# Kernel optimization log

Hardware: AMD Instinct MI355X
Metric: run time of the kernel (lower is better)

## Reference

```python
import jax, jax.numpy as jnp
import numpy as np

B, N = 2, 1024
D, H, DK, L = 128, 8, 16, 4
K_GCN, K_LOC, COARSE = 16, 8, 512
EPS = 1e-5
SCALE = 1.0 / float(np.sqrt(DK))


def _dist2(q, r):
    # squared euclidean distances [Nq, Nr]; same ordering as torch.cdist for topk
    return jnp.sum(q * q, -1)[:, None] - 2.0 * (q @ r.T) + jnp.sum(r * r, -1)[None, :]


def _knn_self(coords, k):
    # knn_graph(loop=False): k nearest neighbors excluding self, per batch
    def one(c):
        d2 = _dist2(c, c) + jnp.eye(c.shape[0], dtype=c.dtype) * 1e10
        return jax.lax.top_k(-d2, k)[1]  # [N, k] source-node indices
    return jax.vmap(one)(coords)


def _gcn(x, idx, w, b, k):
    # PyG GCNConv with self-loops on a knn graph: target in-degree is uniformly k+1,
    # so gcn_norm reduces to mean over {self} U knn neighbors.
    nb = jax.vmap(lambda xb, ib: xb[ib])(x, idx)  # [B,N,k,C]
    agg = (x + nb.sum(2)) / float(k + 1)
    return agg @ w + b


def _ln(x, g, b):
    m = x.mean(-1, keepdims=True)
    v = ((x - m) ** 2).mean(-1, keepdims=True)
    return (x - m) * jax.lax.rsqrt(v + EPS) * g + b


def _neigh_mean(part, pred, k):
    # local_knn + mean over the k gathered partial neighbors
    def one(pb, qb):
        idx = jax.lax.top_k(-_dist2(qb, pb), k)[1]  # [Nq,k]
        return pb[idx].mean(1)                      # [Nq,3]
    return jax.vmap(one)(part, pred)


def _refine(part, pred, sw1, sb1, sw2, sb2, dw, db, cw, cb):
    # LocalRefineStage: seed MLP -> ConvTranspose1d(k=2,s=2) on length-1 seq -> 1x1 conv -> offsets
    nm = _neigh_mean(part, pred, K_LOC)
    comb = jnp.concatenate([pred, nm], -1)                          # [B,N,6]
    seed = jax.nn.relu(comb @ sw1 + sb1) @ sw2 + sb2                # [B,N,128]
    h = jax.nn.relu(jnp.einsum('bnc,cot->bnot', seed, dw) + db[:, None])  # [B,N,128,2]
    y = jnp.einsum('bnot,po->bntp', h, cw) + cb                     # [B,N,2,3]
    child = pred[:, :, None, :] + y
    return child.reshape(pred.shape[0], -1, 3)


def _forward(partial_coords, gcn_w0, gcn_b0, gcn_w1, gcn_b1, enc_fw, enc_fb,
             t_wq, t_bq, t_wk, t_bk, t_wv, t_bv, t_alpha,
             t_f1w, t_f1b, t_f2w, t_f2b, t_ln1g, t_ln1b, t_ln2g, t_ln2b,
             dec_w1, dec_b1, dec_w2, dec_b2,
             st_sw1, st_sb1, st_sw2, st_sb2, st_dw, st_db, st_cw, st_cb):
    coords = partial_coords
    # --- GraphEncoder ---
    idx = _knn_self(coords, K_GCN)
    x = jax.nn.relu(_gcn(coords, idx, gcn_w0, gcn_b0, K_GCN))
    x = jax.nn.relu(_gcn(x, idx, gcn_w1, gcn_b1, K_GCN))
    x = x @ enc_fw + enc_fb  # tokens [B,N,128]; bridge_in is Identity (128==128)
    # --- GeomMultiTokenTransformer ---
    # block-diagonal extraction of (coords coords^T) == per-batch dot-product bias
    G = jnp.einsum('bnc,bmc->bnm', coords, coords)
    for i in range(L):
        q = (x @ t_wq[i] + t_bq[i]).reshape(B, N, H, DK)
        k = (x @ t_wk[i] + t_bk[i]).reshape(B, N, H, DK)
        v = (x @ t_wv[i] + t_bv[i]).reshape(B, N, H, DK)
        scores = jnp.einsum('bnhd,bmhd->bhnm', q, k) * SCALE + (t_alpha[i] * G)[:, None]
        a = jax.nn.softmax(scores, axis=-1)
        attn = jnp.einsum('bhnm,bmhd->bnhd', a, v).reshape(B, N, D)
        x = _ln(x + attn, t_ln1g[i], t_ln1b[i])
        ff = jax.nn.relu(x @ t_f1w[i] + t_f1b[i]) @ t_f2w[i] + t_f2b[i]
        x = _ln(x + ff, t_ln2g[i], t_ln2b[i])
    # --- Snowflake3StageDecoder ---
    gc = x.mean(1)
    pts = (jax.nn.relu(gc @ dec_w1 + dec_b1) @ dec_w2 + dec_b2).reshape(B, COARSE, 3)
    for s in range(3):
        pts = _refine(coords, pts, st_sw1[s], st_sb1[s], st_sw2[s], st_sb2[s],
                      st_dw[s], st_db[s], st_cw[s], st_cb[s])
    return pts  # [B, 4096, 3]


def setup_inputs() -> dict:
    key = jax.random.key(0)
    it = iter(jax.random.split(key, 64))
    def w(*shape):
        return jax.random.normal(next(it), shape, dtype=jnp.float32) * 0.05
    z = lambda *s: jnp.zeros(s, dtype=jnp.float32)
    o = lambda *s: jnp.ones(s, dtype=jnp.float32)
    return {
        'partial_coords': jax.random.normal(next(it), (B, N, 3), dtype=jnp.float32),
        'gcn_w0': w(3, 64), 'gcn_b0': z(64),
        'gcn_w1': w(64, 128), 'gcn_b1': z(128),
        'enc_fw': w(128, 128), 'enc_fb': z(128),
        't_wq': w(L, D, D), 't_bq': z(L, D),
        't_wk': w(L, D, D), 't_bk': z(L, D),
        't_wv': w(L, D, D), 't_bv': z(L, D),
        't_alpha': jnp.full((L,), 0.1, dtype=jnp.float32),
        't_f1w': w(L, D, 4 * D), 't_f1b': z(L, 4 * D),
        't_f2w': w(L, 4 * D, D), 't_f2b': z(L, D),
        't_ln1g': o(L, D), 't_ln1b': z(L, D),
        't_ln2g': o(L, D), 't_ln2b': z(L, D),
        'dec_w1': w(128, 128), 'dec_b1': z(128),
        'dec_w2': w(128, 3 * COARSE), 'dec_b2': z(3 * COARSE),
        'st_sw1': w(3, 6, 128), 'st_sb1': z(3, 128),
        'st_sw2': w(3, 128, 128), 'st_sb2': z(3, 128),
        'st_dw': w(3, 128, 128, 2), 'st_db': z(3, 128),
        'st_cw': w(3, 3, 128), 'st_cb': z(3, 3),
    }


def reference(partial_coords, gcn_w0, gcn_b0, gcn_w1, gcn_b1, enc_fw, enc_fb,
              t_wq, t_bq, t_wk, t_bk, t_wv, t_bv, t_alpha,
              t_f1w, t_f1b, t_f2w, t_f2b, t_ln1g, t_ln1b, t_ln2g, t_ln2b,
              dec_w1, dec_b1, dec_w2, dec_b2,
              st_sw1, st_sb1, st_sw2, st_sb2, st_dw, st_db, st_cw, st_cb):
    return _forward(partial_coords, gcn_w0, gcn_b0, gcn_w1, gcn_b1, enc_fw, enc_fb,
                    t_wq, t_bq, t_wk, t_bk, t_wv, t_bv, t_alpha,
                    t_f1w, t_f1b, t_f2w, t_f2b, t_ln1g, t_ln1b, t_ln2g, t_ln2b,
                    dec_w1, dec_b1, dec_w2, dec_b2,
                    st_sw1, st_sb1, st_sw2, st_sb2, st_dw, st_db, st_cw, st_cb)
```

## Files before the change

### kernel.cpp

```cpp
#include <hip/hip_runtime.h>


#define B_ 2
#define N_ 1024
#define D_ 128
#define H_ 8
#define DK_ 16
#define L_ 4
#define KG_ 16
#define KLOC_ 8
#define COARSE_ 512
#define AW_ 8
#define KSP_ 4
#define PREC_ 17
#define QPL_ 4

static __device__ __forceinline__ float wave_sum(float v) {
    #pragma unroll
    for (int off = 32; off > 0; off >>= 1) v += __shfl_xor(v, off);
    return v;
}
static __device__ __forceinline__ float half_sum(float v) {
    #pragma unroll
    for (int off = 16; off > 0; off >>= 1) v += __shfl_xor(v, off);
    return v;
}

template <int CIN, bool RELU, bool BIAS_HALF>
static __device__ __forceinline__ float4 gemm_body(
        const float* __restrict__ X, const float* __restrict__ W,
        const float* __restrict__ bias, int wstride, int col0) {
    __shared__ float Xs[8 * CIN];
    __shared__ float Ws[64][128];
    int tid = threadIdx.x;
    int row0 = blockIdx.x * 8;
    constexpr int NX4 = 2 * CIN;
    {
        const float4* xg = (const float4*)(X + (size_t)row0 * CIN);
        float4* xs4 = (float4*)Xs;
        #pragma unroll
        for (int i = 0; i < (NX4 + 255) / 256; ++i) {
            int t = tid + i * 256;
            if ((NX4 % 256 == 0) || t < NX4) xs4[t] = xg[t];
        }
    }
    int col4 = (tid & 31) << 2;
    int rowl = tid >> 5;
    float4 acc;
    if (BIAS_HALF) {
        acc.x = bias[(col0 + col4) >> 1];
        acc.y = bias[(col0 + col4 + 1) >> 1];
        acc.z = bias[(col0 + col4 + 2) >> 1];
        acc.w = bias[(col0 + col4 + 3) >> 1];
    } else {
        acc = *(const float4*)(bias + col0 + col4);
    }
    for (int c0 = 0; c0 < CIN; c0 += 64) {
        __syncthreads();
        #pragma unroll
        for (int i = 0; i < 8; ++i) {
            int flat = tid + i * 256;
            int wr = flat >> 5, wc = (flat & 31) << 2;
            *(float4*)&Ws[wr][wc] =
                *(const float4*)(W + (size_t)(c0 + wr) * wstride + col0 + wc);
        }
        __syncthreads();
        const float* xrow = Xs + rowl * CIN + c0;
        #pragma unroll
        for (int c = 0; c < 64; ++c) {
            float xv = xrow[c];
            float4 w = *(const float4*)&Ws[c][col4];
            acc.x += xv * w.x; acc.y += xv * w.y;
            acc.z += xv * w.z; acc.w += xv * w.w;
        }
    }
    if (RELU) {
        acc.x = fmaxf(acc.x, 0.f); acc.y = fmaxf(acc.y, 0.f);
        acc.z = fmaxf(acc.z, 0.f); acc.w = fmaxf(acc.w, 0.f);
    }
    return acc;
}

template <int CIN, bool RELU, bool BIAS_HALF>
__global__ __launch_bounds__(256) void gemm128_kernel(
        const float* __restrict__ X, const float* __restrict__ W,
        const float* __restrict__ bias, float* __restrict__ Y,
        int wstride, int ystride) {
    int col0 = blockIdx.y * 128;
    float4 acc = gemm_body<CIN, RELU, BIAS_HALF>(X, W, bias, wstride, col0);
    int col4 = (threadIdx.x & 31) << 2;
    int row = blockIdx.x * 8 + (threadIdx.x >> 5);
    *(float4*)(Y + (size_t)row * ystride + col0 + col4) = acc;
}

template <int CIN>
__global__ __launch_bounds__(256) void gemm_ln_kernel(
        const float* __restrict__ X, const float* __restrict__ W,
        const float* __restrict__ bias, const float* __restrict__ res,
        const float* __restrict__ g, const float* __restrict__ bt,
        float* __restrict__ Y) {
    float4 acc = gemm_body<CIN, false, false>(X, W, bias, 128, 0);
    int col4 = (threadIdx.x & 31) << 2;
    int row = blockIdx.x * 8 + (threadIdx.x >> 5);
    float4 r = *(const float4*)(res + (size_t)row * D_ + col4);
    acc.x += r.x; acc.y += r.y; acc.z += r.z; acc.w += r.w;
    float mean = half_sum(acc.x + acc.y + acc.z + acc.w) * (1.0f / D_);
    float dx = acc.x - mean, dy = acc.y - mean, dz = acc.z - mean, dw = acc.w - mean;
    float var = half_sum(dx * dx + dy * dy + dz * dz + dw * dw) * (1.0f / D_);
    float rstd = rsqrtf(var + 1e-5f);
    float4 gv = *(const float4*)(g + col4);
    float4 bv = *(const float4*)(bt + col4);
    float4 o;
    o.x = dx * rstd * gv.x + bv.x;
    o.y = dy * rstd * gv.y + bv.y;
    o.z = dz * rstd * gv.z + bv.z;
    o.w = dw * rstd * gv.w + bv.w;
    *(float4*)(Y + (size_t)row * D_ + col4) = o;
}

__global__ __launch_bounds__(256) void gemm_ffn1_kernel(
        const float* __restrict__ pp, const float* __restrict__ xin,
        const float* __restrict__ g, const float* __restrict__ bt,
        const float* __restrict__ W, const float* __restrict__ bias,
        float* __restrict__ xln, float* __restrict__ Y) {
    __shared__ float Xs[8 * 128];
    __shared__ float Ws[64][128];
    int tid = threadIdx.x;
    int row0 = blockIdx.x * 8;
    int col0 = blockIdx.y * 128;
    int col4 = (tid & 31) << 2;
    int rowl = tid >> 5;
    {
        int row = row0 + rowl;
        int b = row >> 10, n = row & (N_ - 1);
        int h = col4 >> 4, d0 = col4 & 15;
        const float* p = pp + (((size_t)(b * 8 + h) * N_ + n) * KSP_) * PREC_;
        float gsum = 0.f, a0 = 0.f, a1 = 0.f, a2 = 0.f, a3 = 0.f;
        #pragma unroll
        for (int s = 0; s < KSP_; ++s) {
            const float* ps = p + s * PREC_;
            gsum += ps[0];
            a0 += ps[1 + d0]; a1 += ps[2 + d0]; a2 += ps[3 + d0]; a3 += ps[4 + d0];
        }
        float inv = 1.0f / gsum;
        float4 xv = *(const float4*)(xin + (size_t)row * D_ + col4);
        float v0 = a0 * inv + xv.x;
        float v1 = a1 * inv + xv.y;
        float v2 = a2 * inv + xv.z;
        float v3 = a3 * inv + xv.w;
        float mean = half_sum(v0 + v1 + v2 + v3) * (1.0f / D_);
        float dx = v0 - mean, dy = v1 - mean, dz = v2 - mean, dw = v3 - mean;
        float var = half_sum(dx * dx + dy * dy + dz * dz + dw * dw) * (1.0f / D_);
        float rstd = rsqrtf(var + 1e-5f);
        float4 gv = *(const float4*)(g + col4);
        float4 bv = *(const float4*)(bt + col4);
        float4 o;
        o.x = dx * rstd * gv.x + bv.x;
        o.y = dy * rstd * gv.y + bv.y;
        o.z = dz * rstd * gv.z + bv.z;
        o.w = dw * rstd * gv.w + bv.w;
        *(float4*)&Xs[rowl * 128 + col4] = o;
        if (blockIdx.y == 0)
            *(float4*)(xln + (size_t)row * D_ + col4) = o;
    }
    float4 acc = *(const float4*)(bias + col0 + col4);
    for (int c0 = 0; c0 < 128; c0 += 64) {
        __syncthreads();
        #pragma unroll
        for (int i = 0; i < 8; ++i) {
            int flat = tid + i * 256;
            int wr = flat >> 5, wc = (flat & 31) << 2;
            *(float4*)&Ws[wr][wc] =
                *(const float4*)(W + (size_t)(c0 + wr) * 512 + col0 + wc);
        }
        __syncthreads();
        const float* xrow = Xs + rowl * 128 + c0;
        #pragma unroll
        for (int c = 0; c < 64; ++c) {
            float xv = xrow[c];
            float4 w = *(const float4*)&Ws[c][col4];
            acc.x += xv * w.x; acc.y += xv * w.y;
            acc.z += xv * w.z; acc.w += xv * w.w;
        }
    }
    acc.x = fmaxf(acc.x, 0.f); acc.y = fmaxf(acc.y, 0.f);
    acc.z = fmaxf(acc.z, 0.f); acc.w = fmaxf(acc.w, 0.f);
    int row = row0 + rowl;
    *(float4*)(Y + (size_t)row * 512 + col0 + col4) = acc;
}

__global__ __launch_bounds__(256) void qkv3_kernel(
        const float* __restrict__ X,
        const float* __restrict__ Wq, const float* __restrict__ bq,
        const float* __restrict__ Wk, const float* __restrict__ bk,
        const float* __restrict__ Wv, const float* __restrict__ bv,
        float* __restrict__ Q, float* __restrict__ K, float* __restrict__ V) {
    const float* W; const float* bias; float* Y;
    if (blockIdx.y == 0)      { W = Wq; bias = bq; Y = Q; }
    else if (blockIdx.y == 1) { W = Wk; bias = bk; Y = K; }
    else                      { W = Wv; bias = bv; Y = V; }
    float4 acc = gemm_body<128, false, false>(X, W, bias, 128, 0);
    int col4 = (threadIdx.x & 31) << 2;
    int row = blockIdx.x * 8 + (threadIdx.x >> 5);
    int b = row >> 10, n = row & (N_ - 1);
    int h = col4 >> 4, d = col4 & 15;
    *(float4*)(Y + (((size_t)(b * 8 + h) * N_ + n) << 4) + d) = acc;
}

__global__ __launch_bounds__(256) void knn_fused_kernel(
        const float* __restrict__ coords, int* __restrict__ knn) {
    __shared__ float4 sc[N_];
    int wid = threadIdx.x >> 6;
    int lane = threadIdx.x & 63;
    size_t q = (size_t)blockIdx.x * 4 + wid;
    int b = (int)(q >> 10), n = (int)(q & (N_ - 1));
    const float* cb = coords + (size_t)b * N_ * 3;
    for (int i = threadIdx.x; i < N_; i += 256) {
        float x = cb[i * 3], y = cb[i * 3 + 1], z = cb[i * 3 + 2];
        sc[i] = make_float4(x, y, z, x * x + y * y + z * z);
    }
    __syncthreads();
    float4 qc = sc[n];
    float qx = qc.x, qy = qc.y, qz = qc.z, q2 = qc.w;
    float ld[16];
    #pragma unroll
    for (int j = 0; j < 16; ++j) {
        int m = (j << 6) | lane;
        float4 c = sc[m];
        float dot = qx * c.x + qy * c.y + qz * c.z;
        float d = (q2 - 2.0f * dot) + c.w;
        ld[j] = (m == n) ? 3e38f : d;
    }
    int* o = knn + q * KG_;
    #pragma unroll
    for (int r = 0; r < KG_; ++r) {
        float dm = ld[0]; int im = lane;
        #pragma unroll
        for (int j = 1; j < 16; ++j) {
            int mj = (j << 6) | lane;
            bool lt = (ld[j] < dm) || (ld[j] == dm && mj < im);
            dm = lt ? ld[j] : dm; im = lt ? mj : im;
        }
        #pragma unroll
        for (int off = 32; off > 0; off >>= 1) {
            float d2 = __shfl_xor(dm, off); int i2 = __shfl_xor(im, off);
            bool lt = (d2 < dm) || (d2 == dm && i2 < im);
            dm = lt ? d2 : dm; im = lt ? i2 : im;
        }
        if (lane == 0) o[r] = im;
        if ((im & 63) == lane) {
            #pragma unroll
            for (int j = 0; j < 16; ++j) if ((im >> 6) == j) ld[j] = 3e38f;
        }
    }
}

__global__ __launch_bounds__(256) void loc_fused_kernel(
        const float* __restrict__ part, const float* __restrict__ pred,
        const float* __restrict__ sw1, const float* __restrict__ sb1,
        float* __restrict__ seedh, int Nq) {
    __shared__ float4 sc[N_];
    int wid = threadIdx.x >> 6;
    int lane = threadIdx.x & 63;
    size_t q = (size_t)blockIdx.x * 4 + wid;
    int b = (int)(q / Nq);
    const float* pb = part + (size_t)b * N_ * 3;
    for (int i = threadIdx.x; i < N_; i += 256) {
        float x = pb[i * 3], y = pb[i * 3 + 1], z = pb[i * 3 + 2];
        sc[i] = make_float4(x, y, z, x * x + y * y + z * z);
    }
    __syncthreads();
    const float* pr = pred + q * 3;
    float qx = pr[0], qy = pr[1], qz = pr[2];
    float q2 = qx * qx + qy * qy + qz * qz;
    float ld[16];
    #pragma unroll
    for (int j = 0; j < 16; ++j) {
        int m = (j << 6) | lane;
        float4 c = sc[m];
        float dot = qx * c.x + qy * c.y + qz * c.z;
        ld[j] = (q2 - 2.0f * dot) + c.w;
    }
    float sx = 0.f, sy = 0.f, sz = 0.f;
    #pragma unroll
    for (int r = 0; r < KLOC_; ++r) {
        float dm = ld[0]; int im = lane;
        #pragma unroll
        for (int j = 1; j < 16; ++j) {
            int mj = (j << 6) | lane;
            bool lt = (ld[j] < dm) || (ld[j] == dm && mj < im);
            dm = lt ? ld[j] : dm; im = lt ? mj : im;
        }
        #pragma unroll
        for (int off = 32; off > 0; off >>= 1) {
            float d2 = __shfl_xor(dm, off); int i2 = __shfl_xor(im, off);
            bool lt = (d2 < dm) || (d2 == dm && i2 < im);
            dm = lt ? d2 : dm; im = lt ? i2 : im;
        }
        float4 w = sc[im];
        sx += w.x; sy += w.y; sz += w.z;
        if ((im & 63) == lane) {
            #pragma unroll
            for (int j = 0; j < 16; ++j) if ((im >> 6) == j) ld[j] = 3e38f;
        }
    }
    float comb[6];
    comb[0] = qx; comb[1] = qy; comb[2] = qz;
    comb[3] = sx * (1.0f / KLOC_);
    comb[4] = sy * (1.0f / KLOC_);
    comb[5] = sz * (1.0f / KLOC_);
    float* so = seedh + q * 128;
    #pragma unroll
    for (int half = 0; half < 2; ++half) {
        int c = lane + half * 64;
        float acc = sb1[c];
        #pragma unroll
        for (int i = 0; i < 6; ++i) acc += comb[i] * sw1[i * 128 + c];
        so[c] = fmaxf(acc, 0.f);
    }
}

__global__ void gcn_agg_kernel(const float* __restrict__ x,
                               const int* __restrict__ knn,
                               float* __restrict__ agg, int C) {
    int i = blockIdx.x * blockDim.x + threadIdx.x;
    if (i >= B_ * N_ * C) return;
    int c = i % C;
    int n = (i / C) % N_;
    int b = i / (C * N_);
    const int* id = knn + ((size_t)b * N_ + n) * KG_;
    float s = x[((size_t)b * N_ + n) * C + c];
    #pragma unroll
    for (int j = 0; j < KG_; ++j) s += x[((size_t)b * N_ + id[j]) * C + c];
    agg[i] = s * (1.0f / (KG_ + 1));
}

template <bool RELU>
__global__ void linear4_kernel(const float* __restrict__ X,
                               const float* __restrict__ W,
                               const float* __restrict__ bias,
                               float* __restrict__ Y,
                               int rows, int Cin, int Cout) {
    int co4 = Cout >> 2;
    int idx = blockIdx.x * blockDim.x + threadIdx.x;
    if (idx >= rows * co4) return;
    int r = idx / co4, o4 = (idx - r * co4) << 2;
    const float* x = X + (size_t)r * Cin;
    float4 acc = *(const float4*)(bias + o4);
    #pragma unroll 4
    for (int c = 0; c < Cin; ++c) {
        float xv = x[c];
        float4 w = *(const float4*)(W + (size_t)c * Cout + o4);
        acc.x += xv * w.x; acc.y += xv * w.y; acc.z += xv * w.z; acc.w += xv * w.w;
    }
    if (RELU) {
        acc.x = fmaxf(acc.x, 0.f); acc.y = fmaxf(acc.y, 0.f);
        acc.z = fmaxf(acc.z, 0.f); acc.w = fmaxf(acc.w, 0.f);
    }
    *(float4*)(Y + (size_t)r * Cout + o4) = acc;
}

__global__ __launch_bounds__(512) void attn_part(
        const float* __restrict__ q,
        const float* __restrict__ k,
        const float* __restrict__ v,
        const float* __restrict__ coords,
        const float* __restrict__ alphap, int layer,
        float* __restrict__ pp) {
    __shared__ float smem[10304];
    float* kst = smem;
    float* vst = smem + 4096;
    float* ssum = smem;
    float* sacc = smem + 2048;
    int bh = blockIdx.x & 15;
    int t = blockIdx.x >> 4;
    int ks = t & (KSP_ - 1);
    int nb = t >> 2;
    int b = bh >> 3;
    int wid = threadIdx.x >> 6;
    int lane = threadIdx.x & 63;
    float alpha = alphap[layer];
    {
        const float4* kg = (const float4*)(k + (((size_t)bh * N_ + ks * 256) << 4));
        const float4* vg = (const float4*)(v + (((size_t)bh * N_ + ks * 256) << 4));
        float4* ks4 = (float4*)kst;
        float4* vs4 = (float4*)vst;
        #pragma unroll
        for (int i = 0; i < 2; ++i) {
            int idx = threadIdx.x + i * 512;
            ks4[idx] = kg[idx];
            vs4[idx] = vg[idx];
        }
    }
    int n0 = nb * 256 + lane;
    const float* cb = coords + (size_t)b * N_ * 3;
    float qv[QPL_][DK_];
    float cx[QPL_], cy[QPL_], cz[QPL_];
    #pragma unroll
    for (int u = 0; u < QPL_; ++u) {
        const float* qp = q + (((size_t)bh * N_ + n0 + u * 64) << 4);
        #pragma unroll
        for (int d = 0; d < DK_; ++d) qv[u][d] = qp[d];
        int nn = n0 + u * 64;
        cx[u] = cb[nn * 3]; cy[u] = cb[nn * 3 + 1]; cz[u] = cb[nn * 3 + 2];
    }
    float sm[QPL_];
    float acc[QPL_][DK_];
    #pragma unroll
    for (int u = 0; u < QPL_; ++u) {
        sm[u] = 0.f;
        #pragma unroll
        for (int d = 0; d < DK_; ++d) acc[u][d] = 0.f;
    }
    __syncthreads();
    int mbase = ks * 256 + wid * 32;
    int lbase = wid * 32;
    #pragma unroll 2
    for (int j = 0; j < 32; ++j) {
        float kk[16];
        {
            const float4* kr = (const float4*)(kst + ((lbase + j) << 4));
            *(float4*)&kk[0] = kr[0]; *(float4*)&kk[4] = kr[1];
            *(float4*)&kk[8] = kr[2]; *(float4*)&kk[12] = kr[3];
        }
        int m = mbase + j;
        float wx = cb[m * 3], wy = cb[m * 3 + 1], wz = cb[m * 3 + 2];
        float p[QPL_];
        #pragma unroll
        for (int u = 0; u < QPL_; ++u) {
            float dot = 0.f;
            #pragma unroll
            for (int d = 0; d < DK_; ++d) dot += qv[u][d] * kk[d];
            p[u] = __expf(dot * 0.25f + alpha * (wx * cx[u] + wy * cy[u] + wz * cz[u]));
            sm[u] += p[u];
        }
        float vv[16];
        {
            const float4* vr = (const float4*)(vst + ((lbase + j) << 4));
            *(float4*)&vv[0] = vr[0]; *(float4*)&vv[4] = vr[1];
            *(float4*)&vv[8] = vr[2]; *(float4*)&vv[12] = vr[3];
        }
        #pragma unroll
        for (int u = 0; u < QPL_; ++u)
            #pragma unroll
            for (int d = 0; d < DK_; ++d) acc[u][d] += p[u] * vv[d];
    }
    __syncthreads();
    #pragma unroll
    for (int u = 0; u < QPL_; ++u) ssum[wid * 256 + u * 64 + lane] = sm[u];
    int qi = threadIdx.x & 63;
    int dq = threadIdx.x >> 6;
    #pragma unroll
    for (int r = 0; r < QPL_; ++r) {
        #pragma unroll
        for (int d = 0; d < DK_; ++d) sacc[lane * 129 + wid * DK_ + d] = acc[r][d];
        __syncthreads();
        int n = nb * 256 + r * 64 + qi;
        float* o = pp + (((size_t)bh * N_ + n) * KSP_ + ks) * PREC_;
        if (dq == 0) {
            float gsum = 0.f;
            #pragma unroll
            for (int w = 0; w < AW_; ++w) gsum += ssum[w * 256 + r * 64 + qi];
            o[0] = gsum;
        }
        #pragma unroll
        for (int dd = 0; dd < 2; ++dd) {
            int d = dq * 2 + dd;
            float a = 0.f;
            #pragma unroll
            for (int w = 0; w < AW_; ++w) a += sacc[qi * 129 + w * DK_ + d];
            o[1 + d] = a;
        }
        __syncthreads();
    }
}

__global__ void colmean_kernel(const float* __restrict__ x,
                               float* __restrict__ gc) {
    int b = blockIdx.x;
    int d = threadIdx.x & 127;
    int sl = threadIdx.x >> 7;
    __shared__ float part[4][128];
    float s = 0.f;
    const float* xb = x + (size_t)b * N_ * D_;
    for (int n = sl * 256; n < sl * 256 + 256; ++n) s += xb[(size_t)n * D_ + d];
    part[sl][d] = s;
    __syncthreads();
    if (sl == 0)
        gc[b * D_ + d] = (part[0][d] + part[1][d] + part[2][d] + part[3][d]) * (1.0f / N_);
}

__global__ void child_kernel(const float* __restrict__ h,
                             const float* __restrict__ cw,
                             const float* __restrict__ cb,
                             const float* __restrict__ pred,
                             float* __restrict__ outp, int Nq) {
    int idx = blockIdx.x * blockDim.x + threadIdx.x;
    if (idx >= B_ * Nq * 6) return;
    int p = idx % 3;
    int t = (idx / 3) & 1;
    int n = (idx / 6) % Nq;
    int b = idx / (6 * Nq);
    const float* hr = h + ((size_t)b * Nq + n) * 256;
    float acc = cb[p];
    #pragma unroll 4
    for (int o = 0; o < 128; ++o) acc += hr[o * 2 + t] * cw[p * 128 + o];
    outp[idx] = pred[((size_t)b * Nq + n) * 3 + p] + acc;
}

static inline int cdiv(int a, int b) { return (a + b - 1) / b; }

extern "C" void kernel_launch(void* const* d_in, const int* in_sizes, int n_in,
                              void* d_out, int out_size, void* d_ws, size_t ws_size,
                              hipStream_t stream) {
    (void)in_sizes; (void)n_in; (void)out_size; (void)ws_size;
    const float* coords = (const float*)d_in[0];
    const float* gcn_w0 = (const float*)d_in[1];
    const float* gcn_b0 = (const float*)d_in[2];
    const float* gcn_w1 = (const float*)d_in[3];
    const float* gcn_b1 = (const float*)d_in[4];
    const float* enc_fw = (const float*)d_in[5];
    const float* enc_fb = (const float*)d_in[6];
    const float* t_wq   = (const float*)d_in[7];
    const float* t_bq   = (const float*)d_in[8];
    const float* t_wk   = (const float*)d_in[9];
    const float* t_bk   = (const float*)d_in[10];
    const float* t_wv   = (const float*)d_in[11];
    const float* t_bv   = (const float*)d_in[12];
    const float* t_alpha= (const float*)d_in[13];
    const float* t_f1w  = (const float*)d_in[14];
    const float* t_f1b  = (const float*)d_in[15];
    const float* t_f2w  = (const float*)d_in[16];
    const float* t_f2b  = (const float*)d_in[17];
    const float* t_ln1g = (const float*)d_in[18];
    const float* t_ln1b = (const float*)d_in[19];
    const float* t_ln2g = (const float*)d_in[20];
    const float* t_ln2b = (const float*)d_in[21];
    const float* dec_w1 = (const float*)d_in[22];
    const float* dec_b1 = (const float*)d_in[23];
    const float* dec_w2 = (const float*)d_in[24];
    const float* dec_b2 = (const float*)d_in[25];
    const float* st_sw1 = (const float*)d_in[26];
    const float* st_sb1 = (const float*)d_in[27];
    const float* st_sw2 = (const float*)d_in[28];
    const float* st_sb2 = (const float*)d_in[29];
    const float* st_dw  = (const float*)d_in[30];
    const float* st_db  = (const float*)d_in[31];
    const float* st_cw  = (const float*)d_in[32];
    const float* st_cb  = (const float*)d_in[33];
    float* out = (float*)d_out;

    char* ws = (char*)d_ws;
    size_t off = 0;
    auto alloc = [&](size_t bytes) -> void* {
        void* p = ws + off;
        off += (bytes + 255) & ~(size_t)255;
        return p;
    };
    int*   knn   = (int*)  alloc((size_t)B_ * N_ * KG_ * 4);
    float* app   = (float*)alloc((size_t)B_ * H_ * N_ * KSP_ * PREC_ * 4);
    float* agg   = (float*)alloc((size_t)B_ * N_ * 64 * 4);
    float* x64   = (float*)alloc((size_t)B_ * N_ * 64 * 4);
    float* xb    = (float*)alloc((size_t)B_ * N_ * D_ * 4);
    float* x     = (float*)alloc((size_t)B_ * N_ * D_ * 4);
    float* q     = (float*)alloc((size_t)B_ * N_ * D_ * 4);
    float* k     = (float*)alloc((size_t)B_ * N_ * D_ * 4);
    float* v     = (float*)alloc((size_t)B_ * N_ * D_ * 4);
    float* ffh   = (float*)alloc((size_t)B_ * N_ * 512 * 4);
    float* gc    = (float*)alloc((size_t)B_ * D_ * 4);
    float* dech  = (float*)alloc((size_t)B_ * D_ * 4);
    float* pts0  = (float*)alloc((size_t)B_ * COARSE_ * 3 * 4);
    float* pts1  = (float*)alloc((size_t)B_ * 1024 * 3 * 4);
    float* pts2  = (float*)alloc((size_t)B_ * 2048 * 3 * 4);
    float* seedh = (float*)alloc((size_t)B_ * 2048 * 128 * 4);
    float* seed  = (float*)alloc((size_t)B_ * 2048 * 128 * 4);
    float* hb    = (float*)alloc((size_t)B_ * 2048 * 256 * 4);

    const int rows = B_ * N_;

    knn_fused_kernel<<<rows / 4, 256, 0, stream>>>(coords, knn);
    gcn_agg_kernel<<<cdiv(rows * 3, 256), 256, 0, stream>>>(coords, knn, agg, 3);
    linear4_kernel<true><<<cdiv(rows * 16, 256), 256, 0, stream>>>(agg, gcn_w0, gcn_b0, x64, rows, 3, 64);
    gcn_agg_kernel<<<cdiv(rows * 64, 256), 256, 0, stream>>>(x64, knn, agg, 64);
    gemm128_kernel<64, true, false><<<dim3(rows / 8, 1), 256, 0, stream>>>(agg, gcn_w1, gcn_b1, xb, 128, 128);
    gemm128_kernel<128, false, false><<<dim3(rows / 8, 1), 256, 0, stream>>>(xb, enc_fw, enc_fb, x, 128, 128);

    for (int i = 0; i < L_; ++i) {
        qkv3_kernel<<<dim3(rows / 8, 3), 256, 0, stream>>>(
            x, t_wq + i * 16384, t_bq + i * 128, t_wk + i * 16384, t_bk + i * 128,
            t_wv + i * 16384, t_bv + i * 128, q, k, v);
        attn_part<<<B_ * H_ * (N_ / 256) * KSP_, 512, 0, stream>>>(q, k, v, coords, t_alpha, i, app);
        gemm_ffn1_kernel<<<dim3(rows / 8, 4), 256, 0, stream>>>(
            app, x, t_ln1g + i * 128, t_ln1b + i * 128,
            t_f1w + i * 128 * 512, t_f1b + i * 512, xb, ffh);
        gemm_ln_kernel<512><<<rows / 8, 256, 0, stream>>>(ffh, t_f2w + i * 512 * 128, t_f2b + i * 128, xb, t_ln2g + i * 128, t_ln2b + i * 128, x);
    }

    colmean_kernel<<<B_, 512, 0, stream>>>(x, gc);
    linear4_kernel<true><<<cdiv(B_ * 32, 256), 256, 0, stream>>>(gc, dec_w1, dec_b1, dech, B_, 128, 128);
    linear4_kernel<false><<<cdiv(B_ * 384, 256), 256, 0, stream>>>(dech, dec_w2, dec_b2, pts0, B_, 128, 1536);

    const float* pred = pts0;
    float* outs[3] = { pts1, pts2, out };
    int Nq = COARSE_;
    for (int s = 0; s < 3; ++s) {
        int srows = B_ * Nq;
        loc_fused_kernel<<<srows / 4, 256, 0, stream>>>(
            coords, pred, st_sw1 + s * 6 * 128, st_sb1 + s * 128, seedh, Nq);
        gemm128_kernel<128, false, false><<<dim3(srows / 8, 1), 256, 0, stream>>>(seedh, st_sw2 + s * 128 * 128, st_sb2 + s * 128, seed, 128, 128);
        gemm128_kernel<128, true, true><<<dim3(srows / 8, 2), 256, 0, stream>>>(seed, st_dw + s * 128 * 256, st_db + s * 128, hb, 256, 256);
        child_kernel<<<cdiv(srows * 6, 256), 256, 0, stream>>>(hb, st_cw + s * 3 * 128, st_cb + s * 3, pred, outs[s], Nq);
        pred = outs[s];
        Nq <<= 1;
    }
}
```

Before: 422.4 us.

## Fuse GCN aggregation, decoder MLP and refine-stage tail into fewer kernels

Folds the GCN neighbor aggregation into the following linear layers: a per-row kernel for the 3-to-64 layer, and aggregation into shared memory ahead of the 64-to-128 GEMM. The two decoder linear layers merge into one kernel. The refine-stage 1x1 GEMM, transposed-conv GEMM and child offset computation become one kernel that keeps intermediates in shared memory. This removes many launches and global round trips for the agg, seed and hb buffers, at the cost of more shared memory per block and recomputing the decoder's first layer in every block.

```diff
diff --git a/kernel.cpp b/kernel.cpp
--- a/kernel.cpp
+++ b/kernel.cpp
@@ -91,6 +91,74 @@
     int col4 = (threadIdx.x & 31) << 2;
     int row = blockIdx.x * 8 + (threadIdx.x >> 5);
     *(float4*)(Y + (size_t)row * ystride + col0 + col4) = acc;
+}
+
+__global__ __launch_bounds__(256) void gemm_gcn_kernel(
+        const float* __restrict__ x64, const int* __restrict__ knn,
+        const float* __restrict__ W, const float* __restrict__ bias,
+        float* __restrict__ Y) {
+    __shared__ float Xs[8 * 64];
+    __shared__ float Ws[64][128];
+    int tid = threadIdx.x;
+    int row0 = blockIdx.x * 8;
+    #pragma unroll
+    for (int i = 0; i < 2; ++i) {
+        int idx = tid + i * 256;
+        int r = idx >> 6, c = idx & 63;
+        int row = row0 + r;
+        int b = row >> 10;
+        const int* id = knn + (size_t)row * KG_;
+        float val = x64[(size_t)row * 64 + c];
+        #pragma unroll
+        for (int j = 0; j < KG_; ++j)
+            val += x64[((size_t)(b << 10) + id[j]) * 64 + c];
+        Xs[idx] = val * (1.0f / (KG_ + 1));
+    }
+    int col4 = (tid & 31) << 2;
+    int rowl = tid >> 5;
+    float4 acc = *(const float4*)(bias + col4);
+    __syncthreads();
+    #pragma unroll
+    for (int i = 0; i < 8; ++i) {
+        int flat = tid + i * 256;
+        int wr = flat >> 5, wc = (flat & 31) << 2;
+        *(float4*)&Ws[wr][wc] = *(const float4*)(W + (size_t)wr * 128 + wc);
+    }
+    __syncthreads();
+    const float* xrow = Xs + rowl * 64;
+    #pragma unroll
+    for (int c = 0; c < 64; ++c) {
+        float xv = xrow[c];
+        float4 w = *(const float4*)&Ws[c][col4];
+        acc.x += xv * w.x; acc.y += xv * w.y;
+        acc.z += xv * w.z; acc.w += xv * w.w;
+    }
+    acc.x = fmaxf(acc.x, 0.f); acc.y = fmaxf(acc.y, 0.f);
+    acc.z = fmaxf(acc.z, 0.f); acc.w = fmaxf(acc.w, 0.f);
+    int row = row0 + rowl;
+    *(float4*)(Y + (size_t)row * 128 + col4) = acc;
+}
+
+__global__ __launch_bounds__(256) void gcnlin0_kernel(
+        const float* __restrict__ coords, const int* __restrict__ knn,
+        const float* __restrict__ w0, const float* __restrict__ b0,
+        float* __restrict__ x64) {
+    int lane = threadIdx.x & 63;
+    int row = blockIdx.x * 4 + (threadIdx.x >> 6);
+    int b = row >> 10;
+    const float* cb = coords + (size_t)(b << 10) * 3;
+    int n = row & (N_ - 1);
+    float ax = cb[n * 3], ay = cb[n * 3 + 1], az = cb[n * 3 + 2];
+    const int* id = knn + (size_t)row * KG_;
+    #pragma unroll
+    for (int j = 0; j < KG_; ++j) {
+        int m = id[j];
+        ax += cb[m * 3]; ay += cb[m * 3 + 1]; az += cb[m * 3 + 2];
+    }
+    float s = 1.0f / (KG_ + 1);
+    ax *= s; ay *= s; az *= s;
+    float acc = b0[lane] + ax * w0[lane] + ay * w0[64 + lane] + az * w0[128 + lane];
+    x64[(size_t)row * 64 + lane] = fmaxf(acc, 0.f);
 }
 
 template <int CIN>
@@ -320,44 +388,116 @@
     }
 }
 
-__global__ void gcn_agg_kernel(const float* __restrict__ x,
-                               const int* __restrict__ knn,
-                               float* __restrict__ agg, int C) {
-    int i = blockIdx.x * blockDim.x + threadIdx.x;
-    if (i >= B_ * N_ * C) return;
-    int c = i % C;
-    int n = (i / C) % N_;
-    int b = i / (C * N_);
-    const int* id = knn + ((size_t)b * N_ + n) * KG_;
-    float s = x[((size_t)b * N_ + n) * C + c];
-    #pragma unroll
-    for (int j = 0; j < KG_; ++j) s += x[((size_t)b * N_ + id[j]) * C + c];
-    agg[i] = s * (1.0f / (KG_ + 1));
-}
-
-template <bool RELU>
-__global__ void linear4_kernel(const float* __restrict__ X,
-                               const float* __restrict__ W,
-                               const float* __restrict__ bias,
-                               float* __restrict__ Y,
-                               int rows, int Cin, int Cout) {
-    int co4 = Cout >> 2;
-    int idx = blockIdx.x * blockDim.x + threadIdx.x;
-    if (idx >= rows * co4) return;
-    int r = idx / co4, o4 = (idx - r * co4) << 2;
-    const float* x = X + (size_t)r * Cin;
-    float4 acc = *(const float4*)(bias + o4);
+__global__ __launch_bounds__(256) void refine_tail_kernel(
+        const float* __restrict__ seedh,
+        const float* __restrict__ sw2, const float* __restrict__ sb2,
+        const float* __restrict__ dw, const float* __restrict__ db,
+        const float* __restrict__ cw, const float* __restrict__ cb,
+        const float* __restrict__ pred, float* __restrict__ outp) {
+    __shared__ float Xs[8 * 128];
+    __shared__ float Ws[64][128];
+    __shared__ float Sd[8 * 128];
+    __shared__ float Hb[8 * 256];
+    int tid = threadIdx.x;
+    int row0 = blockIdx.x * 8;
+    int col4 = (tid & 31) << 2;
+    int rowl = tid >> 5;
+    {
+        const float4* xg = (const float4*)(seedh + (size_t)row0 * 128);
+        float4* xs4 = (float4*)Xs;
+        xs4[tid] = xg[tid];
+    }
+    float4 acc = *(const float4*)(sb2 + col4);
+    for (int c0 = 0; c0 < 128; c0 += 64) {
+        __syncthreads();
+        #pragma unroll
+        for (int i = 0; i < 8; ++i) {
+            int flat = tid + i * 256;
+            int wr = flat >> 5, wc = (flat & 31) << 2;
+            *(float4*)&Ws[wr][wc] =
+                *(const float4*)(sw2 + (size_t)(c0 + wr) * 128 + wc);
+        }
+        __syncthreads();
+        const float* xrow = Xs + rowl * 128 + c0;
+        #pragma unroll
+        for (int c = 0; c < 64; ++c) {
+            float xv = xrow[c];
+            float4 w = *(const float4*)&Ws[c][col4];
+            acc.x += xv * w.x; acc.y += xv * w.y;
+            acc.z += xv * w.z; acc.w += xv * w.w;
+        }
+    }
+    __syncthreads();
+    *(float4*)&Sd[rowl * 128 + col4] = acc;
+    #pragma unroll
+    for (int panel = 0; panel < 2; ++panel) {
+        int col0 = panel * 128;
+        float4 a2;
+        a2.x = db[(col0 + col4) >> 1];
+        a2.y = db[(col0 + col4 + 1) >> 1];
+        a2.z = db[(col0 + col4 + 2) >> 1];
+        a2.w = db[(col0 + col4 + 3) >> 1];
+        for (int c0 = 0; c0 < 128; c0 += 64) {
+            __syncthreads();
+            #pragma unroll
+            for (int i = 0; i < 8; ++i) {
+                int flat = tid + i * 256;
+                int wr = flat >> 5, wc = (flat & 31) << 2;
+                *(float4*)&Ws[wr][wc] =
+                    *(const float4*)(dw + (size_t)(c0 + wr) * 256 + col0 + wc);
+            }
+            __syncthreads();
+            const float* xrow = Sd + rowl * 128 + c0;
+            #pragma unroll
+            for (int c = 0; c < 64; ++c) {
+                float xv = xrow[c];
+                float4 w = *(const float4*)&Ws[c][col4];
+                a2.x += xv * w.x; a2.y += xv * w.y;
+                a2.z += xv * w.z; a2.w += xv * w.w;
+            }
+        }
+        a2.x = fmaxf(a2.x, 0.f); a2.y = fmaxf(a2.y, 0.f);
+        a2.z = fmaxf(a2.z, 0.f); a2.w = fmaxf(a2.w, 0.f);
+        __syncthreads();
+        *(float4*)&Hb[rowl * 256 + col0 + col4] = a2;
+    }
+    __syncthreads();
+    if (tid < 48) {
+        int r = tid / 6, rem = tid % 6;
+        int t = rem / 3, p = rem % 3;
+        const float* hr = Hb + r * 256;
+        float a = cb[p];
+        #pragma unroll 4
+        for (int o = 0; o < 128; ++o) a += hr[o * 2 + t] * cw[p * 128 + o];
+        size_t row = row0 + r;
+        outp[row * 6 + t * 3 + p] = pred[row * 3 + p] + a;
+    }
+}
+
+__global__ __launch_bounds__(256) void dec12_kernel(
+        const float* __restrict__ gc,
+        const float* __restrict__ w1, const float* __restrict__ b1,
+        const float* __restrict__ w2, const float* __restrict__ b2,
+        float* __restrict__ pts0) {
+    __shared__ float gcs[128];
+    __shared__ float dech[128];
+    int tid = threadIdx.x;
+    int row = blockIdx.x / 6;
+    int colb = (blockIdx.x % 6) * 256;
+    if (tid < 128) gcs[tid] = gc[row * 128 + tid];
+    __syncthreads();
+    if (tid < 128) {
+        float a = b1[tid];
+        #pragma unroll 4
+        for (int c = 0; c < 128; ++c) a += gcs[c] * w1[c * 128 + tid];
+        dech[tid] = fmaxf(a, 0.f);
+    }
+    __syncthreads();
+    int col = colb + tid;
+    float a = b2[col];
     #pragma unroll 4
-    for (int c = 0; c < Cin; ++c) {
-        float xv = x[c];
-        float4 w = *(const float4*)(W + (size_t)c * Cout + o4);
-        acc.x += xv * w.x; acc.y += xv * w.y; acc.z += xv * w.z; acc.w += xv * w.w;
-    }
-    if (RELU) {
-        acc.x = fmaxf(acc.x, 0.f); acc.y = fmaxf(acc.y, 0.f);
-        acc.z = fmaxf(acc.z, 0.f); acc.w = fmaxf(acc.w, 0.f);
-    }
-    *(float4*)(Y + (size_t)r * Cout + o4) = acc;
+    for (int c = 0; c < 128; ++c) a += dech[c] * w2[(size_t)c * 1536 + col];
+    pts0[(size_t)row * 1536 + col] = a;
 }
 
 __global__ __launch_bounds__(512) void attn_part(
@@ -488,24 +628,6 @@
     __syncthreads();
     if (sl == 0)
         gc[b * D_ + d] = (part[0][d] + part[1][d] + part[2][d] + part[3][d]) * (1.0f / N_);
-}
-
-__global__ void child_kernel(const float* __restrict__ h,
-                             const float* __restrict__ cw,
-                             const float* __restrict__ cb,
-                             const float* __restrict__ pred,
-                             float* __restrict__ outp, int Nq) {
-    int idx = blockIdx.x * blockDim.x + threadIdx.x;
-    if (idx >= B_ * Nq * 6) return;
-    int p = idx % 3;
-    int t = (idx / 3) & 1;
-    int n = (idx / 6) % Nq;
-    int b = idx / (6 * Nq);
-    const float* hr = h + ((size_t)b * Nq + n) * 256;
-    float acc = cb[p];
-    #pragma unroll 4
-    for (int o = 0; o < 128; ++o) acc += hr[o * 2 + t] * cw[p * 128 + o];
-    outp[idx] = pred[((size_t)b * Nq + n) * 3 + p] + acc;
 }
 
 static inline int cdiv(int a, int b) { return (a + b - 1) / b; }
@@ -559,7 +681,6 @@
     };
     int*   knn   = (int*)  alloc((size_t)B_ * N_ * KG_ * 4);
     float* app   = (float*)alloc((size_t)B_ * H_ * N_ * KSP_ * PREC_ * 4);
-    float* agg   = (float*)alloc((size_t)B_ * N_ * 64 * 4);
     float* x64   = (float*)alloc((size_t)B_ * N_ * 64 * 4);
     float* xb    = (float*)alloc((size_t)B_ * N_ * D_ * 4);
     float* x     = (float*)alloc((size_t)B_ * N_ * D_ * 4);
@@ -568,21 +689,16 @@
     float* v     = (float*)alloc((size_t)B_ * N_ * D_ * 4);
     float* ffh   = (float*)alloc((size_t)B_ * N_ * 512 * 4);
     float* gc    = (float*)alloc((size_t)B_ * D_ * 4);
-    float* dech  = (float*)alloc((size_t)B_ * D_ * 4);
     float* pts0  = (float*)alloc((size_t)B_ * COARSE_ * 3 * 4);
     float* pts1  = (float*)alloc((size_t)B_ * 1024 * 3 * 4);
     float* pts2  = (float*)alloc((size_t)B_ * 2048 * 3 * 4);
     float* seedh = (float*)alloc((size_t)B_ * 2048 * 128 * 4);
-    float* seed  = (float*)alloc((size_t)B_ * 2048 * 128 * 4);
-    float* hb    = (float*)alloc((size_t)B_ * 2048 * 256 * 4);
 
     const int rows = B_ * N_;
 
     knn_fused_kernel<<<rows / 4, 256, 0, stream>>>(coords, knn);
-    gcn_agg_kernel<<<cdiv(rows * 3, 256), 256, 0, stream>>>(coords, knn, agg, 3);
-    linear4_kernel<true><<<cdiv(rows * 16, 256), 256, 0, stream>>>(agg, gcn_w0, gcn_b0, x64, rows, 3, 64);
-    gcn_agg_kernel<<<cdiv(rows * 64, 256), 256, 0, stream>>>(x64, knn, agg, 64);
-    gemm128_kernel<64, true, false><<<dim3(rows / 8, 1), 256, 0, stream>>>(agg, gcn_w1, gcn_b1, xb, 128, 128);
+    gcnlin0_kernel<<<rows / 4, 256, 0, stream>>>(coords, knn, gcn_w0, gcn_b0, x64);
+    gemm_gcn_kernel<<<rows / 8, 256, 0, stream>>>(x64, knn, gcn_w1, gcn_b1, xb);
     gemm128_kernel<128, false, false><<<dim3(rows / 8, 1), 256, 0, stream>>>(xb, enc_fw, enc_fb, x, 128, 128);
 
     for (int i = 0; i < L_; ++i) {
@@ -597,8 +713,7 @@
     }
 
     colmean_kernel<<<B_, 512, 0, stream>>>(x, gc);
-    linear4_kernel<true><<<cdiv(B_ * 32, 256), 256, 0, stream>>>(gc, dec_w1, dec_b1, dech, B_, 128, 128);
-    linear4_kernel<false><<<cdiv(B_ * 384, 256), 256, 0, stream>>>(dech, dec_w2, dec_b2, pts0, B_, 128, 1536);
+    dec12_kernel<<<12, 256, 0, stream>>>(gc, dec_w1, dec_b1, dec_w2, dec_b2, pts0);
 
     const float* pred = pts0;
     float* outs[3] = { pts1, pts2, out };
@@ -607,9 +722,10 @@
         int srows = B_ * Nq;
         loc_fused_kernel<<<srows / 4, 256, 0, stream>>>(
             coords, pred, st_sw1 + s * 6 * 128, st_sb1 + s * 128, seedh, Nq);
-        gemm128_kernel<128, false, false><<<dim3(srows / 8, 1), 256, 0, stream>>>(seedh, st_sw2 + s * 128 * 128, st_sb2 + s * 128, seed, 128, 128);
-        gemm128_kernel<128, true, true><<<dim3(srows / 8, 2), 256, 0, stream>>>(seed, st_dw + s * 128 * 256, st_db + s * 128, hb, 256, 256);
-        child_kernel<<<cdiv(srows * 6, 256), 256, 0, stream>>>(hb, st_cw + s * 3 * 128, st_cb + s * 3, pred, outs[s], Nq);
+        refine_tail_kernel<<<srows / 8, 256, 0, stream>>>(
+            seedh, st_sw2 + s * 128 * 128, st_sb2 + s * 128,
+            st_dw + s * 128 * 256, st_db + s * 128,
+            st_cw + s * 3 * 128, st_cb + s * 3, pred, outs[s]);
         pred = outs[s];
         Nq <<= 1;
     }
```

After: 380.7 us. -9.9%, faster.
